# Kernel tuning notes

Hardware: AMD Instinct MI355X
Metric: run time of the kernel (lower is better)

The kernel has to match this reference:

```python
import jax, jax.numpy as jnp
import numpy as np

B, S, D = 16, 4096, 64


def setup_inputs() -> dict:
    key = jax.random.key(0)
    kq, kk, kv = jax.random.split(key, 3)
    q = jax.random.normal(kq, (B, S, D), dtype=jnp.float32)
    k = jax.random.normal(kk, (B, S, D), dtype=jnp.float32)
    v = jax.random.normal(kv, (B, S, D), dtype=jnp.float32)
    inv_scale_factor = jnp.float32(1.0 / np.sqrt(D))  # source DIVIDES by this
    p = 0  # dropout prob (deterministic baseline -> identity)
    return {"q": q, "k": k, "v": v, "inv_scale_factor": inv_scale_factor, "p": p}


def reference(q, k, v, inv_scale_factor, p):
    # qk = q @ k^T ; scaled = qk / inv_scale_factor (faithful to source)
    scores = jnp.einsum("bsd,btd->bst", q, k) / inv_scale_factor  # [B,S,S]
    attn = jax.nn.softmax(scores, axis=-1)
    # dropout with p=0 is identity (eval-mode baseline)
    out = jnp.einsum("bst,btd->bsd", attn, v)  # [B,S,D]
    return out
```

## Files before the change

### kernel.cpp

```cpp
#include <hip/hip_runtime.h>
#include <hip/hip_bf16.h>

typedef float f32x4 __attribute__((ext_vector_type(4)));
typedef float f32x16 __attribute__((ext_vector_type(16)));
typedef _Float16 half8 __attribute__((ext_vector_type(8)));
typedef __bf16 bf16x8 __attribute__((ext_vector_type(8)));
typedef __bf16 bf16x4 __attribute__((ext_vector_type(4)));
typedef unsigned short ushort_t;

constexpr int Bb = 16, Ss = 4096, Dd = 64;
constexpr int KBLK = 32, QBLK = 64;
constexpr int NT = Ss / KBLK;
constexpr float kLOG2E = 1.44269504088896340736f;
constexpr float DEFER_THR = 10.0f;

constexpr int KP_BLOCKS = (Bb * Ss * Dd / 8) / 256;
constexpr int VT_BLOCKS = (Bb * Dd * (Ss / 32)) / 256;

#define GLOAD_LDS16(gp, lp)                                                              \
    __builtin_amdgcn_global_load_lds(                                                    \
        (const __attribute__((address_space(1))) void*)(gp),                             \
        (__attribute__((address_space(3))) void*)(lp), 16, 0, 0)

__global__ __launch_bounds__(256)
void prep_f16s(const float* __restrict__ K, const float* __restrict__ V,
               _Float16* __restrict__ Khi, _Float16* __restrict__ Klo,
               _Float16* __restrict__ Vt)
{
    const int bid = blockIdx.x;
    if (bid < KP_BLOCKS) {
        const size_t idx = ((size_t)bid * 256 + threadIdx.x) * 8;
        const float4 a = *reinterpret_cast<const float4*>(K + idx);
        const float4 c = *reinterpret_cast<const float4*>(K + idx + 4);
        float xs[8] = {a.x, a.y, a.z, a.w, c.x, c.y, c.z, c.w};
        half8 h8, l8;
#pragma unroll
        for (int i = 0; i < 8; ++i) {
            const _Float16 h = (_Float16)xs[i];
            h8[i] = h;
            l8[i] = (_Float16)(xs[i] - (float)h);
        }
        *reinterpret_cast<half8*>(Khi + idx) = h8;
        *reinterpret_cast<half8*>(Klo + idx) = l8;
    } else {
        const int t = (bid - KP_BLOCKS) * 256 + threadIdx.x;
        const int d = t & 63;
        const int s32 = (t >> 6) & (Ss / 32 - 1);
        const int b = t >> 13;
        const float* vp = V + ((size_t)b * Ss + (size_t)s32 * 32) * Dd + d;
        __align__(16) _Float16 ob[32];
#pragma unroll
        for (int j = 0; j < 32; ++j) ob[j] = (_Float16)vp[(size_t)j * Dd];
        _Float16* op = Vt + ((size_t)b * Dd + d) * Ss + (size_t)s32 * 32;
#pragma unroll
        for (int j8 = 0; j8 < 4; ++j8)
            *reinterpret_cast<half8*>(op + j8 * 8) = *reinterpret_cast<half8*>(ob + j8 * 8);
    }
}

__global__ __launch_bounds__(256, 3)
void attn_fwd_v4(const float* __restrict__ Q, const float* __restrict__ inv_scale,
                 const _Float16* __restrict__ Khi, const _Float16* __restrict__ Klo,
                 const _Float16* __restrict__ Vt, float* __restrict__ Out)
{
    __shared__ __align__(16) unsigned char smem[50 * 1024];

    const int tid = threadIdx.x;
    const int lane = tid & 63;
    const int w = tid >> 6;
    const int p = w & 1;
    const int qg = w >> 1;
    const int l31 = lane & 31;
    const int hi = lane >> 5;

    const int bid = (blockIdx.x & 7) * 128 + (blockIdx.x >> 3);
    const int b = bid >> 6;
    const int q0 = (bid & 63) * QBLK;

    const _Float16* KhB = Khi + (size_t)b * Ss * Dd;
    const _Float16* KlB = Klo + (size_t)b * Ss * Dd;
    const _Float16* VB = Vt + (size_t)b * Dd * Ss;

    const int kk = tid >> 3;
    const int ksrc = kk * Dd + (((tid & 7) ^ (kk & 7)) << 3);
    const int dd_ = tid >> 2;
    const size_t vsrc = (size_t)dd_ * Ss + (((tid & 3) ^ (dd_ & 3)) << 3);

#define STAGE(t)                                                                            \
    do {                                                                                    \
        const int _sl = (t) & 3;                                                            \
        GLOAD_LDS16(KhB + (size_t)(t) * (KBLK * Dd) + ksrc, smem + _sl * 4096 + tid * 16);  \
        GLOAD_LDS16(KlB + (size_t)(t) * (KBLK * Dd) + ksrc,                                 \
                    smem + 16384 + _sl * 4096 + tid * 16);                                  \
        GLOAD_LDS16(VB + (size_t)(t) * KBLK + vsrc, smem + 32768 + _sl * 4096 + tid * 16);  \
    } while (0)

    STAGE(0);
    STAGE(1);

    int koff[4], voff[4];
#pragma unroll
    for (int ks = 0; ks < 4; ++ks)
        koff[ks] = l31 * 128 + ((((ks << 1) + hi) ^ (l31 & 7)) << 4);
#pragma unroll
    for (int i = 0; i < 4; ++i) {
        const int d = (i >> 1) * 32 + l31;
        voff[i] = d * 64 + (((((i & 1) << 1) + hi) ^ (d & 3)) << 4);
    }

    union H8 { half8 h; unsigned int u[4]; };
    H8 qhi[4], qlo[4];
    {
        const float s2 = (1.0f / inv_scale[0]) * kLOG2E;
        const float* qrow = Q + ((size_t)b * Ss + q0 + qg * 32 + l31) * Dd;
#pragma unroll
        for (int ks = 0; ks < 4; ++ks) {
            const int d0 = ks * 16 + hi * 8;
            const float4 a = *reinterpret_cast<const float4*>(qrow + d0);
            const float4 c = *reinterpret_cast<const float4*>(qrow + d0 + 4);
            float xs[8] = {a.x, a.y, a.z, a.w, c.x, c.y, c.z, c.w};
#pragma unroll
            for (int i = 0; i < 8; ++i) {
                const float x = xs[i] * s2;
                const _Float16 h = (_Float16)x;
                qhi[ks].h[i] = h;
                qlo[ks].h[i] = (_Float16)(x - (float)h);
            }
        }
    }

    f32x16 O0, O1;
#pragma unroll
    for (int r = 0; r < 16; ++r) { O0[r] = 0.f; O1[r] = 0.f; }
    float m_run = -INFINITY, l_run = 0.f;

    __syncthreads();

    for (int it = 0; it < NT / 2; ++it) {
        const int t = 2 * it + p;
        const unsigned char* khbase = smem + (t & 3) * 4096;
        const unsigned char* klbase = smem + 16384 + (t & 3) * 4096;
        const unsigned char* vbase = smem + 32768 + (t & 3) * 4096;

        if (it < NT / 2 - 1) { STAGE(2 * it + 2); STAGE(2 * it + 3); }

        f32x16 S;
#pragma unroll
        for (int r = 0; r < 16; ++r) S[r] = 0.f;
#pragma unroll
        for (int ks = 0; ks < 4; ++ks) {
            const half8 kh = *reinterpret_cast<const half8*>(khbase + koff[ks]);
            const half8 kl = *reinterpret_cast<const half8*>(klbase + koff[ks]);
            S = __builtin_amdgcn_mfma_f32_32x32x16_f16(kh, qhi[ks].h, S, 0, 0, 0);
            S = __builtin_amdgcn_mfma_f32_32x32x16_f16(kl, qhi[ks].h, S, 0, 0, 0);
            S = __builtin_amdgcn_mfma_f32_32x32x16_f16(kh, qlo[ks].h, S, 0, 0, 0);
        }

        float tmax = S[0];
#pragma unroll
        for (int r = 1; r < 16; ++r) tmax = fmaxf(tmax, S[r]);
        tmax = fmaxf(tmax, __shfl_xor(tmax, 32));

        float fac = 1.0f;
        if (__any(tmax > m_run + DEFER_THR)) {
            const float m_new = fmaxf(m_run, tmax);
            fac = __builtin_amdgcn_exp2f(m_run - m_new);
            m_run = m_new;
#pragma unroll
            for (int r = 0; r < 16; ++r) { O0[r] *= fac; O1[r] *= fac; }
        }

        float tsum = 0.f;
#pragma unroll
        for (int r = 0; r < 16; ++r) {
            S[r] = __builtin_amdgcn_exp2f(S[r] - m_run);
            tsum += S[r];
        }
        tsum += __shfl_xor(tsum, 32);
        l_run = l_run * fac + tsum;

        unsigned int wd[8];
#pragma unroll
        for (int j = 0; j < 8; ++j) {
            const auto h2 = __builtin_amdgcn_cvt_pkrtz(S[2 * j], S[2 * j + 1]);
            wd[j] = __builtin_bit_cast(unsigned int, h2);
        }
        auto xhalf = [&](unsigned int& a, unsigned int& c) {
            const unsigned int y = hi ? a : c;
            const unsigned int sy = __shfl_xor(y, 32);
            const unsigned int na = hi ? sy : a;
            const unsigned int nc = hi ? c : sy;
            a = na; c = nc;
        };
        xhalf(wd[0], wd[2]);
        xhalf(wd[1], wd[3]);
        xhalf(wd[4], wd[6]);
        xhalf(wd[5], wd[7]);

        H8 pf0, pf1;
        pf0.u[0] = wd[0]; pf0.u[1] = wd[1]; pf0.u[2] = wd[2]; pf0.u[3] = wd[3];
        pf1.u[0] = wd[4]; pf1.u[1] = wd[5]; pf1.u[2] = wd[6]; pf1.u[3] = wd[7];

        O0 = __builtin_amdgcn_mfma_f32_32x32x16_f16(
            *reinterpret_cast<const half8*>(vbase + voff[0]), pf0.h, O0, 0, 0, 0);
        O0 = __builtin_amdgcn_mfma_f32_32x32x16_f16(
            *reinterpret_cast<const half8*>(vbase + voff[1]), pf1.h, O0, 0, 0, 0);
        O1 = __builtin_amdgcn_mfma_f32_32x32x16_f16(
            *reinterpret_cast<const half8*>(vbase + voff[2]), pf0.h, O1, 0, 0, 0);
        O1 = __builtin_amdgcn_mfma_f32_32x32x16_f16(
            *reinterpret_cast<const half8*>(vbase + voff[3]), pf1.h, O1, 0, 0, 0);

        __syncthreads();
    }

    float* mO = (float*)smem;
    float* ml = (float*)(smem + 49152);

    if (p == 1) {
#pragma unroll
        for (int dblk = 0; dblk < 2; ++dblk)
#pragma unroll
            for (int rr = 0; rr < 4; ++rr) {
                f32x4 v;
                if (dblk == 0) {
                    v[0] = O0[rr * 4 + 0]; v[1] = O0[rr * 4 + 1];
                    v[2] = O0[rr * 4 + 2]; v[3] = O0[rr * 4 + 3];
                } else {
                    v[0] = O1[rr * 4 + 0]; v[1] = O1[rr * 4 + 1];
                    v[2] = O1[rr * 4 + 2]; v[3] = O1[rr * 4 + 3];
                }
                *reinterpret_cast<f32x4*>(mO + (((qg * 2 + dblk) * 4 + rr) << 8) + lane * 4) = v;
            }
        if (hi == 0) {
            ml[qg * 64 + l31] = m_run;
            ml[qg * 64 + 32 + l31] = l_run;
        }
    }
    __syncthreads();
    if (p == 0) {
        const float m1 = ml[qg * 64 + l31];
        const float l1 = ml[qg * 64 + 32 + l31];
        const float mm = fmaxf(m_run, m1);
        float f0 = __builtin_amdgcn_exp2f(m_run - mm);
        float f1 = __builtin_amdgcn_exp2f(m1 - mm);
        const float inv = 1.0f / (l_run * f0 + l1 * f1);
        f0 *= inv; f1 *= inv;
        float* orow = Out + ((size_t)b * Ss + q0 + qg * 32 + l31) * Dd;
#pragma unroll
        for (int dblk = 0; dblk < 2; ++dblk)
#pragma unroll
            for (int rr = 0; rr < 4; ++rr) {
                const f32x4 ov = *reinterpret_cast<const f32x4*>(
                    mO + (((qg * 2 + dblk) * 4 + rr) << 8) + lane * 4);
                f32x4 res;
#pragma unroll
                for (int j = 0; j < 4; ++j) {
                    const float mine = (dblk == 0) ? O0[rr * 4 + j] : O1[rr * 4 + j];
                    res[j] = mine * f0 + ov[j] * f1;
                }
                *reinterpret_cast<f32x4*>(orow + dblk * 32 + rr * 8 + hi * 4) = res;
            }
    }
#undef STAGE
}

__global__ __launch_bounds__(256)
void attn_fwd_fallback(const float* __restrict__ Q, const float* __restrict__ K,
                       const float* __restrict__ V, const float* __restrict__ inv_scale,
                       float* __restrict__ Out)
{
    __shared__ __align__(16) ushort_t sKhi[KBLK * Dd];
    __shared__ __align__(16) ushort_t sKlo[KBLK * Dd];
    __shared__ __align__(16) ushort_t sVt[Dd * KBLK];
    __shared__ __align__(16) ushort_t sP[4][16 * KBLK];

    const int tid = threadIdx.x;
    const int lane = tid & 63;
    const int w = tid >> 6;
    const int q15 = lane & 15;
    const int g = lane >> 4;
    const int b = blockIdx.x >> 6;
    const int q0 = (blockIdx.x & 63) * QBLK;
    const float scale = 1.0f / inv_scale[0];

    const float* qptr = Q + (((size_t)b * Ss) + q0 + w * 16 + q15) * Dd;
    bf16x8 qhi[2], qlo[2];
#pragma unroll
    for (int ds = 0; ds < 2; ++ds) {
        const float4 f0 = *reinterpret_cast<const float4*>(qptr + ds * 32 + g * 8);
        const float4 f1 = *reinterpret_cast<const float4*>(qptr + ds * 32 + g * 8 + 4);
        float xs[8] = {f0.x, f0.y, f0.z, f0.w, f1.x, f1.y, f1.z, f1.w};
#pragma unroll
        for (int i = 0; i < 8; ++i) {
            __bf16 h = (__bf16)xs[i];
            qhi[ds][i] = h;
            qlo[ds][i] = (__bf16)(xs[i] - (float)h);
        }
    }
    const int krs = tid >> 3;
    const int kc8 = (tid & 7) * 8;
    const int kidx = krs * Dd + (kc8 ^ ((krs & 7) << 3));
    const float* kbase = K + ((size_t)b * Ss) * Dd;
    const int vd = tid & 63;
    const int vk8 = (tid >> 6) * 8;
    const int vidx = vd * KBLK + (vk8 ^ ((vd & 3) << 3));
    const float* vbase = V + ((size_t)b * Ss) * Dd;

    f32x4 Oacc[4];
#pragma unroll
    for (int dt = 0; dt < 4; ++dt)
#pragma unroll
        for (int r = 0; r < 4; ++r) Oacc[dt][r] = 0.f;
    float m_run = -INFINITY, l_run = 0.f;

    for (int k0 = 0; k0 < Ss; k0 += KBLK) {
        {
            const float* p0 = kbase + (size_t)(k0 + krs) * Dd + kc8;
            const float4 a = *reinterpret_cast<const float4*>(p0);
            const float4 c = *reinterpret_cast<const float4*>(p0 + 4);
            float xs[8] = {a.x, a.y, a.z, a.w, c.x, c.y, c.z, c.w};
            bf16x8 h8, l8;
#pragma unroll
            for (int i = 0; i < 8; ++i) {
                __bf16 h = (__bf16)xs[i];
                h8[i] = h;
                l8[i] = (__bf16)(xs[i] - (float)h);
            }
            *reinterpret_cast<bf16x8*>(&sKhi[kidx]) = h8;
            *reinterpret_cast<bf16x8*>(&sKlo[kidx]) = l8;
        }
        {
            bf16x8 v8;
#pragma unroll
            for (int j = 0; j < 8; ++j) v8[j] = (__bf16)vbase[(size_t)(k0 + vk8 + j) * Dd + vd];
            *reinterpret_cast<bf16x8*>(&sVt[vidx]) = v8;
        }
        __syncthreads();

        float z[2][4];
#pragma unroll
        for (int t = 0; t < 2; ++t) {
            const int krow = t * 16 + q15;
            f32x4 acc;
            acc[0] = acc[1] = acc[2] = acc[3] = 0.f;
#pragma unroll
            for (int ds = 0; ds < 2; ++ds) {
                const int ci = (ds * 32 + g * 8) ^ ((krow & 7) << 3);
                const bf16x8 kh = *reinterpret_cast<const bf16x8*>(&sKhi[krow * Dd + ci]);
                const bf16x8 kl = *reinterpret_cast<const bf16x8*>(&sKlo[krow * Dd + ci]);
                acc = __builtin_amdgcn_mfma_f32_16x16x32_bf16(kh, qhi[ds], acc, 0, 0, 0);
                acc = __builtin_amdgcn_mfma_f32_16x16x32_bf16(kl, qhi[ds], acc, 0, 0, 0);
                acc = __builtin_amdgcn_mfma_f32_16x16x32_bf16(kh, qlo[ds], acc, 0, 0, 0);
            }
#pragma unroll
            for (int r = 0; r < 4; ++r) z[t][r] = acc[r] * scale;
        }

        float tmax = z[0][0];
#pragma unroll
        for (int t = 0; t < 2; ++t)
#pragma unroll
            for (int r = 0; r < 4; ++r) tmax = fmaxf(tmax, z[t][r]);
        tmax = fmaxf(tmax, __shfl_xor(tmax, 16));
        tmax = fmaxf(tmax, __shfl_xor(tmax, 32));
        const float m_new = fmaxf(m_run, tmax);

        float pz[2][4];
        float tsum = 0.f;
#pragma unroll
        for (int t = 0; t < 2; ++t)
#pragma unroll
            for (int r = 0; r < 4; ++r) {
                const float e = __builtin_amdgcn_exp2f((z[t][r] - m_new) * kLOG2E);
                pz[t][r] = e;
                tsum += e;
            }
        tsum += __shfl_xor(tsum, 16);
        tsum += __shfl_xor(tsum, 32);
        const float fac = __builtin_amdgcn_exp2f((m_run - m_new) * kLOG2E);
        l_run = l_run * fac + tsum;
        m_run = m_new;

#pragma unroll
        for (int t = 0; t < 2; ++t) {
            bf16x4 pb;
#pragma unroll
            for (int r = 0; r < 4; ++r) pb[r] = (__bf16)pz[t][r];
            const int pidx = q15 * KBLK + ((t * 16 + g * 4) ^ ((q15 & 3) << 3));
            *reinterpret_cast<bf16x4*>(&sP[w][pidx]) = pb;
        }
        {
            const float fr0 = __shfl(fac, g * 4 + 0);
            const float fr1 = __shfl(fac, g * 4 + 1);
            const float fr2 = __shfl(fac, g * 4 + 2);
            const float fr3 = __shfl(fac, g * 4 + 3);
#pragma unroll
            for (int dt = 0; dt < 4; ++dt) {
                Oacc[dt][0] *= fr0; Oacc[dt][1] *= fr1;
                Oacc[dt][2] *= fr2; Oacc[dt][3] *= fr3;
            }
        }
        const int paidx = q15 * KBLK + ((g * 8) ^ ((q15 & 3) << 3));
        const bf16x8 pa = *reinterpret_cast<const bf16x8*>(&sP[w][paidx]);
#pragma unroll
        for (int dt = 0; dt < 4; ++dt) {
            const int dd = dt * 16 + q15;
            const bf16x8 vf =
                *reinterpret_cast<const bf16x8*>(&sVt[dd * KBLK + ((g * 8) ^ ((dd & 3) << 3))]);
            Oacc[dt] = __builtin_amdgcn_mfma_f32_16x16x32_bf16(pa, vf, Oacc[dt], 0, 0, 0);
        }
        __syncthreads();
    }

    const float invl = 1.0f / l_run;
    float il[4];
#pragma unroll
    for (int r = 0; r < 4; ++r) il[r] = __shfl(invl, g * 4 + r);
    float* obase = Out + (((size_t)b * Ss) + q0 + w * 16) * Dd;
#pragma unroll
    for (int dt = 0; dt < 4; ++dt)
#pragma unroll
        for (int r = 0; r < 4; ++r)
            obase[(size_t)(g * 4 + r) * Dd + dt * 16 + q15] = Oacc[dt][r] * il[r];
}

extern "C" void kernel_launch(void* const* d_in, const int* in_sizes, int n_in,
                              void* d_out, int out_size, void* d_ws, size_t ws_size,
                              hipStream_t stream)
{
    const float* q = (const float*)d_in[0];
    const float* k = (const float*)d_in[1];
    const float* v = (const float*)d_in[2];
    const float* inv_scale = (const float*)d_in[3];
    float* out = (float*)d_out;
    (void)in_sizes; (void)n_in; (void)out_size;

    const size_t NKV = (size_t)Bb * Ss * Dd;
    const size_t need = NKV * 3 * sizeof(_Float16);

    if (ws_size >= need) {
        _Float16* Khi = (_Float16*)d_ws;
        _Float16* Klo = Khi + NKV;
        _Float16* Vt = Klo + NKV;
        hipLaunchKernelGGL(prep_f16s, dim3(KP_BLOCKS + VT_BLOCKS), dim3(256), 0, stream,
                           k, v, Khi, Klo, Vt);
        hipLaunchKernelGGL(attn_fwd_v4, dim3(Bb * (Ss / QBLK)), dim3(256), 0, stream,
                           q, inv_scale, Khi, Klo, Vt, out);
    } else {
        hipLaunchKernelGGL(attn_fwd_fallback, dim3(Bb * (Ss / QBLK)), dim3(256), 0, stream,
                           q, k, v, inv_scale, out);
    }
}
```

Before: 195.5 us.

## Double query tile to 128 rows with 512-thread blocks sharing K/V stages

Raises the query block from 64 to 128 rows and launches 512-thread blocks. Eight waves now consume each staged K/V tile, so every K and V byte loaded into LDS is reused across twice as many queries. The async global-to-LDS staging is split by role: the first 256 threads load Khi/Klo and the rest load Vt. Block-index swizzling and the epilogue LDS offsets are updated to match. The trade-offs are a tighter register budget from the launch bound of 4 waves per EU, with possible spills, and half as many blocks in the grid.

```diff
diff --git a/kernel.cpp b/kernel.cpp
--- a/kernel.cpp
+++ b/kernel.cpp
@@ -9,7 +9,7 @@
 typedef unsigned short ushort_t;
 
 constexpr int Bb = 16, Ss = 4096, Dd = 64;
-constexpr int KBLK = 32, QBLK = 64;
+constexpr int KBLK = 32, QBLK = 128;
 constexpr int NT = Ss / KBLK;
 constexpr float kLOG2E = 1.44269504088896340736f;
 constexpr float DEFER_THR = 10.0f;
@@ -58,12 +58,12 @@
     }
 }
 
-__global__ __launch_bounds__(256, 3)
-void attn_fwd_v4(const float* __restrict__ Q, const float* __restrict__ inv_scale,
+__global__ __launch_bounds__(512, 4)
+void attn_fwd_v5(const float* __restrict__ Q, const float* __restrict__ inv_scale,
                  const _Float16* __restrict__ Khi, const _Float16* __restrict__ Klo,
                  const _Float16* __restrict__ Vt, float* __restrict__ Out)
 {
-    __shared__ __align__(16) unsigned char smem[50 * 1024];
+    __shared__ __align__(16) unsigned char smem[48 * 1024];
 
     const int tid = threadIdx.x;
     const int lane = tid & 63;
@@ -73,26 +73,32 @@
     const int l31 = lane & 31;
     const int hi = lane >> 5;
 
-    const int bid = (blockIdx.x & 7) * 128 + (blockIdx.x >> 3);
-    const int b = bid >> 6;
-    const int q0 = (bid & 63) * QBLK;
+    const int bid = (blockIdx.x & 7) * 64 + (blockIdx.x >> 3);
+    const int b = bid >> 5;
+    const int q0 = (bid & 31) * QBLK;
 
     const _Float16* KhB = Khi + (size_t)b * Ss * Dd;
     const _Float16* KlB = Klo + (size_t)b * Ss * Dd;
     const _Float16* VB = Vt + (size_t)b * Dd * Ss;
 
-    const int kk = tid >> 3;
-    const int ksrc = kk * Dd + (((tid & 7) ^ (kk & 7)) << 3);
-    const int dd_ = tid >> 2;
-    const size_t vsrc = (size_t)dd_ * Ss + (((tid & 3) ^ (dd_ & 3)) << 3);
+    const int c = tid & 255;
+    const int kk = c >> 3;
+    const int ksrc = kk * Dd + (((c & 7) ^ (kk & 7)) << 3);
+    const int dd_ = c >> 2;
+    const size_t vsrc = (size_t)dd_ * Ss + (((c & 3) ^ (dd_ & 3)) << 3);
 
 #define STAGE(t)                                                                            \
     do {                                                                                    \
         const int _sl = (t) & 3;                                                            \
-        GLOAD_LDS16(KhB + (size_t)(t) * (KBLK * Dd) + ksrc, smem + _sl * 4096 + tid * 16);  \
-        GLOAD_LDS16(KlB + (size_t)(t) * (KBLK * Dd) + ksrc,                                 \
-                    smem + 16384 + _sl * 4096 + tid * 16);                                  \
-        GLOAD_LDS16(VB + (size_t)(t) * KBLK + vsrc, smem + 32768 + _sl * 4096 + tid * 16);  \
+        if (tid < 256) {                                                                    \
+            GLOAD_LDS16(KhB + (size_t)(t) * (KBLK * Dd) + ksrc,                             \
+                        smem + _sl * 4096 + c * 16);                                        \
+            GLOAD_LDS16(KlB + (size_t)(t) * (KBLK * Dd) + ksrc,                             \
+                        smem + 16384 + _sl * 4096 + c * 16);                                \
+        } else {                                                                            \
+            GLOAD_LDS16(VB + (size_t)(t) * KBLK + vsrc,                                     \
+                        smem + 32768 + _sl * 4096 + c * 16);                                \
+        }                                                                                   \
     } while (0)
 
     STAGE(0);
@@ -117,8 +123,8 @@
         for (int ks = 0; ks < 4; ++ks) {
             const int d0 = ks * 16 + hi * 8;
             const float4 a = *reinterpret_cast<const float4*>(qrow + d0);
-            const float4 c = *reinterpret_cast<const float4*>(qrow + d0 + 4);
-            float xs[8] = {a.x, a.y, a.z, a.w, c.x, c.y, c.z, c.w};
+            const float4 cc = *reinterpret_cast<const float4*>(qrow + d0 + 4);
+            float xs[8] = {a.x, a.y, a.z, a.w, cc.x, cc.y, cc.z, cc.w};
 #pragma unroll
             for (int i = 0; i < 8; ++i) {
                 const float x = xs[i] * s2;
@@ -185,12 +191,12 @@
             const auto h2 = __builtin_amdgcn_cvt_pkrtz(S[2 * j], S[2 * j + 1]);
             wd[j] = __builtin_bit_cast(unsigned int, h2);
         }
-        auto xhalf = [&](unsigned int& a, unsigned int& c) {
-            const unsigned int y = hi ? a : c;
+        auto xhalf = [&](unsigned int& a, unsigned int& cx) {
+            const unsigned int y = hi ? a : cx;
             const unsigned int sy = __shfl_xor(y, 32);
             const unsigned int na = hi ? sy : a;
-            const unsigned int nc = hi ? c : sy;
-            a = na; c = nc;
+            const unsigned int nc = hi ? cx : sy;
+            a = na; cx = nc;
         };
         xhalf(wd[0], wd[2]);
         xhalf(wd[1], wd[3]);
@@ -214,7 +220,7 @@
     }
 
     float* mO = (float*)smem;
-    float* ml = (float*)(smem + 49152);
+    float* ml = (float*)(smem + 32768);
 
     if (p == 1) {
 #pragma unroll
@@ -280,7 +286,7 @@
     const int q15 = lane & 15;
     const int g = lane >> 4;
     const int b = blockIdx.x >> 6;
-    const int q0 = (blockIdx.x & 63) * QBLK;
+    const int q0 = (blockIdx.x & 63) * 64;
     const float scale = 1.0f / inv_scale[0];
 
     const float* qptr = Q + (((size_t)b * Ss) + q0 + w * 16 + q15) * Dd;
@@ -444,10 +450,10 @@
         _Float16* Vt = Klo + NKV;
         hipLaunchKernelGGL(prep_f16s, dim3(KP_BLOCKS + VT_BLOCKS), dim3(256), 0, stream,
                            k, v, Khi, Klo, Vt);
-        hipLaunchKernelGGL(attn_fwd_v4, dim3(Bb * (Ss / QBLK)), dim3(256), 0, stream,
+        hipLaunchKernelGGL(attn_fwd_v5, dim3(Bb * (Ss / QBLK)), dim3(512), 0, stream,
                            q, inv_scale, Khi, Klo, Vt, out);
     } else {
-        hipLaunchKernelGGL(attn_fwd_fallback, dim3(Bb * (Ss / QBLK)), dim3(256), 0, stream,
+        hipLaunchKernelGGL(attn_fwd_fallback, dim3(Bb * 64), dim3(256), 0, stream,
                            q, k, v, inv_scale, out);
     }
 }
```

New measurement: 170.5 us. 1.15x faster.
